# Optimization experiments

Measured on AMD Instinct MI355X. Metric: run time of the kernel, lower is better.

## Reference

```python
import math
import jax, jax.numpy as jnp
import numpy as np

N_HEAD = 12
LN_EPS = 1e-5

def _gelu(x):
    # NewGELU: tanh approximation
    c = math.sqrt(2.0 / math.pi)
    return 0.5 * x * (1.0 + jnp.tanh(c * (x + 0.044715 * x ** 3)))

def _ln(x, w, b):
    m = x.mean(-1, keepdims=True)
    v = x.var(-1, keepdims=True)
    return (x - m) / jnp.sqrt(v + LN_EPS) * w + b

def setup_inputs() -> dict:
    key = jax.random.key(0)
    ks = jax.random.split(key, 8)
    L, C, V, BS = 12, 768, 30522, 1024
    B, T = 4, 1024
    std = 0.02
    inp = {
        'idx': jax.random.randint(ks[0], (B, T), 0, V),
        'wte': jax.random.normal(ks[1], (V, C), jnp.float32) * std,
        'wpe': jax.random.normal(ks[2], (BS, C), jnp.float32) * std,
        'ln1_w': jnp.ones((L, C), jnp.float32),
        'ln1_b': jnp.zeros((L, C), jnp.float32),
        'attn_w': jax.random.normal(ks[3], (L, 3 * C, C), jnp.float32) * std,
        'attn_b': jnp.zeros((L, 3 * C), jnp.float32),
        'proj_w': jax.random.normal(ks[4], (L, C, C), jnp.float32) * (std / math.sqrt(2 * L)),
        'proj_b': jnp.zeros((L, C), jnp.float32),
        'ln2_w': jnp.ones((L, C), jnp.float32),
        'ln2_b': jnp.zeros((L, C), jnp.float32),
        'fc_w': jax.random.normal(ks[5], (L, 4 * C, C), jnp.float32) * std,
        'fc_b': jnp.zeros((L, 4 * C), jnp.float32),
        'mproj_w': jax.random.normal(ks[6], (L, C, 4 * C), jnp.float32) * (std / math.sqrt(2 * L)),
        'mproj_b': jnp.zeros((L, C), jnp.float32),
        'lnf_w': jnp.ones((C,), jnp.float32),
        'lnf_b': jnp.zeros((C,), jnp.float32),
        'lm_head_w': jax.random.normal(ks[7], (V, C), jnp.float32) * std,
    }
    return inp

def reference(idx, wte, wpe, ln1_w, ln1_b, attn_w, attn_b, proj_w, proj_b,
              ln2_w, ln2_b, fc_w, fc_b, mproj_w, mproj_b, lnf_w, lnf_b, lm_head_w):
    B, T = idx.shape
    C = wte.shape[1]
    H = N_HEAD
    D = C // H
    scale = 1.0 / math.sqrt(D)
    x = wte[idx] + wpe[:T][None]  # [B,T,C], drop is identity (p=0)

    def block(x, p):
        l1w, l1b, aw, ab, pw, pb, l2w, l2b, fw, fb, mw, mb = p
        h = _ln(x, l1w, l1b)
        qkv = jnp.einsum('btc,ec->bte', h, aw) + ab  # [B,T,3C]
        q, k, v = jnp.split(qkv, 3, axis=-1)
        q = q.reshape(B, T, H, D)
        k = k.reshape(B, T, H, D)
        v = v.reshape(B, T, H, D)
        att = jnp.einsum('bthd,bshd->bhts', q, k) * scale  # [B,H,T,T]
        att = jax.nn.softmax(att, axis=-1)  # mask=None: full attention
        y = jnp.einsum('bhts,bshd->bthd', att, v).reshape(B, T, C)
        x = x + jnp.einsum('btc,oc->bto', y, pw) + pb
        h = _gelu(jnp.einsum('btc,fc->btf', _ln(x, l2w, l2b), fw) + fb)
        x = x + jnp.einsum('btf,cf->btc', h, mw) + mb
        return x, None

    x, _ = jax.lax.scan(block, x, (ln1_w, ln1_b, attn_w, attn_b, proj_w, proj_b,
                                   ln2_w, ln2_b, fc_w, fc_b, mproj_w, mproj_b))
    x = _ln(x, lnf_w, lnf_b)
    logits = jnp.einsum('btc,vc->btv', x, lm_head_w)  # [B,T,V]
    return logits
```

## Files before the change

### kernel.cpp

```cpp
#include <hip/hip_runtime.h>
#include <hip/hip_bf16.h>
#include <math.h>

typedef __attribute__((ext_vector_type(8))) short short8;
typedef __attribute__((ext_vector_type(4))) float f32x4;

typedef unsigned short u16;

__device__ __forceinline__ u16 f2bf(float f) {
    union { float f; unsigned int u; } v; v.f = f;
    unsigned int u = v.u;
    unsigned int r = (u + 0x7fffu + ((u >> 16) & 1u)) >> 16;
    return (u16)r;
}
__device__ __forceinline__ float bf2f(u16 u) {
    union { unsigned int u; float f; } v; v.u = ((unsigned int)u) << 16;
    return v.f;
}

__device__ __forceinline__ void gload16(const void* g, void* l) {
    __builtin_amdgcn_global_load_lds(
        (const __attribute__((address_space(1))) void*)g,
        (__attribute__((address_space(3))) void*)l, 16, 0, 0);
}

__global__ __launch_bounds__(256) void castw_kernel(const float* __restrict__ src,
                                                    u16* __restrict__ dst,
                                                    long n, long npad) {
    long i = ((long)blockIdx.x * 256 + threadIdx.x) * 4;
    const long stride = (long)gridDim.x * 1024;
    for (; i < npad; i += stride) {
        ushort4 o;
        if (i < n) {
            float4 v = *reinterpret_cast<const float4*>(src + i);
            o.x = f2bf(v.x); o.y = f2bf(v.y); o.z = f2bf(v.z); o.w = f2bf(v.w);
        } else {
            o = make_ushort4(0, 0, 0, 0);
        }
        *reinterpret_cast<ushort4*>(dst + i) = o;
    }
}

__global__ __launch_bounds__(256) void embed_kernel(const int* __restrict__ idx,
                                                    const float* __restrict__ wte,
                                                    const float* __restrict__ wpe,
                                                    float* __restrict__ x) {
    const int row = blockIdx.x;
    const int tid = threadIdx.x;
    const int t = row & 1023;
    const int tok = idx[row];
    const float* we = wte + (size_t)tok * 768;
    const float* pe = wpe + (size_t)t * 768;
    float* xr = x + (size_t)row * 768;
    xr[tid]       = we[tid]       + pe[tid];
    xr[tid + 256] = we[tid + 256] + pe[tid + 256];
    xr[tid + 512] = we[tid + 512] + pe[tid + 512];
}

__global__ __launch_bounds__(256) void ln_kernel(const float* __restrict__ x,
                                                 const float* __restrict__ w,
                                                 const float* __restrict__ b,
                                                 u16* __restrict__ out) {
    const int row = blockIdx.x;
    const int tid = threadIdx.x;
    const float* xr = x + (size_t)row * 768;
    float v0 = xr[tid], v1 = xr[tid + 256], v2 = xr[tid + 512];
    float s = v0 + v1 + v2;
    float q = v0 * v0 + v1 * v1 + v2 * v2;
    #pragma unroll
    for (int off = 32; off >= 1; off >>= 1) {
        s += __shfl_xor(s, off);
        q += __shfl_xor(q, off);
    }
    __shared__ float rs[4], rq[4];
    const int wid = tid >> 6, lane = tid & 63;
    if (lane == 0) { rs[wid] = s; rq[wid] = q; }
    __syncthreads();
    s = rs[0] + rs[1] + rs[2] + rs[3];
    q = rq[0] + rq[1] + rq[2] + rq[3];
    const float mean = s * (1.f / 768.f);
    const float var = q * (1.f / 768.f) - mean * mean;
    const float rstd = rsqrtf(var + 1e-5f);
    u16* orow = out + (size_t)row * 768;
    orow[tid]       = f2bf((v0 - mean) * rstd * w[tid]       + b[tid]);
    orow[tid + 256] = f2bf((v1 - mean) * rstd * w[tid + 256] + b[tid + 256]);
    orow[tid + 512] = f2bf((v2 - mean) * rstd * w[tid + 512] + b[tid + 512]);
}

template<int EPI>
__global__ __launch_bounds__(256) void gemm_bb(
        const u16* __restrict__ A, int lda,
        const u16* __restrict__ B, int ldb,
        const float* __restrict__ bias,
        void* __restrict__ Cout, int ldc,
        int N, int K, int nmt,
        float* __restrict__ resid) {
    __shared__ __align__(16) u16 lds[2][2][128 * 32];
    const int tid = threadIdx.x;
    const int lane = tid & 63, wid = tid >> 6;
    const int nwg = gridDim.x;
    const int o = blockIdx.x;
    const int wg = (o & 7) * (nwg >> 3) + (o >> 3);
    const int m0 = (wg % nmt) * 128, n0 = (wg / nmt) * 128;

    const int wm = (wid >> 1) * 64, wn = (wid & 1) * 64;
    const int l16 = lane & 15, lk = (lane >> 4) * 8;

    const size_t a_off0 = (size_t)(m0 + (tid >> 2)) * lda + (tid & 3) * 8;
    const size_t a_off1 = a_off0 + (size_t)64 * lda;
    const size_t b_off0 = (size_t)(n0 + (tid >> 2)) * ldb + (tid & 3) * 8;
    const size_t b_off1 = b_off0 + (size_t)64 * ldb;

    f32x4 acc[4][4];
    #pragma unroll
    for (int i = 0; i < 4; i++)
        #pragma unroll
        for (int j = 0; j < 4; j++)
            acc[i][j] = (f32x4){0.f, 0.f, 0.f, 0.f};

    const int nk = K >> 5;
    {
        u16* As = lds[0][0]; u16* Bs = lds[0][1];
        gload16(A + a_off0, As + tid * 8);
        gload16(A + a_off1, As + tid * 8 + 2048);
        gload16(B + b_off0, Bs + tid * 8);
        gload16(B + b_off1, Bs + tid * 8 + 2048);
    }
    for (int t = 0; t < nk; ++t) {
        if (t + 1 < nk) {
            u16* As = lds[(t + 1) & 1][0]; u16* Bs = lds[(t + 1) & 1][1];
            const int k0 = (t + 1) << 5;
            gload16(A + a_off0 + k0, As + tid * 8);
            gload16(A + a_off1 + k0, As + tid * 8 + 2048);
            gload16(B + b_off0 + k0, Bs + tid * 8);
            gload16(B + b_off1 + k0, Bs + tid * 8 + 2048);
            asm volatile("s_waitcnt vmcnt(4)" ::: "memory");
        } else {
            asm volatile("s_waitcnt vmcnt(0)" ::: "memory");
        }
        __builtin_amdgcn_s_barrier();
        asm volatile("" ::: "memory");
        const u16* As = lds[t & 1][0];
        const u16* Bs = lds[t & 1][1];
        short8 af[4], bf[4];
        #pragma unroll
        for (int i = 0; i < 4; i++) {
            af[i] = *reinterpret_cast<const short8*>(&As[(wm + i * 16 + l16) * 32 + lk]);
            bf[i] = *reinterpret_cast<const short8*>(&Bs[(wn + i * 16 + l16) * 32 + lk]);
        }
        #pragma unroll
        for (int mi = 0; mi < 4; mi++)
            #pragma unroll
            for (int ni = 0; ni < 4; ni++)
                acc[mi][ni] = __builtin_amdgcn_mfma_f32_16x16x32_bf16(af[mi], bf[ni], acc[mi][ni], 0, 0, 0);
        asm volatile("" ::: "memory");
        __builtin_amdgcn_s_barrier();
    }

    if (EPI == 3) {
        float* ct = reinterpret_cast<float*>(&lds[0][0][0]) + wid * 1024;
        const int rw = (lane >> 4) * 4;
        const int rr = lane >> 2;
        const int rc = (lane & 3) * 16;
        #pragma unroll
        for (int mi = 0; mi < 4; mi++) {
            asm volatile("" ::: "memory");
            #pragma unroll
            for (int ni = 0; ni < 4; ni++)
                #pragma unroll
                for (int j = 0; j < 4; j++)
                    ct[(rw + j) * 64 + ni * 16 + l16] = acc[mi][ni][j];
            asm volatile("" ::: "memory");
            const int m = m0 + wm + mi * 16 + rr;
            const int nb = n0 + wn + rc;
            float* crow = (float*)Cout + (size_t)m * ldc + nb;
            #pragma unroll
            for (int q = 0; q < 4; q++) {
                const float4 v = *reinterpret_cast<const float4*>(&ct[rr * 64 + rc + q * 4]);
                if (nb + q * 4 + 3 < N) {
                    *reinterpret_cast<float4*>(crow + q * 4) = v;
                } else {
                    const float vv[4] = {v.x, v.y, v.z, v.w};
                    #pragma unroll
                    for (int e = 0; e < 4; e++)
                        if (nb + q * 4 + e < N) crow[q * 4 + e] = vv[e];
                }
            }
        }
    } else {
        const int cb = n0 + wn + l16;
        const int rb = m0 + wm + (lane >> 4) * 4;
        #pragma unroll
        for (int ni = 0; ni < 4; ni++) {
            const int n = cb + ni * 16;
            const float bv = bias[n];
            #pragma unroll
            for (int mi = 0; mi < 4; mi++) {
                #pragma unroll
                for (int j = 0; j < 4; j++) {
                    const int m = rb + mi * 16 + j;
                    float v = acc[mi][ni][j] + bv;
                    if (EPI == 0) {
                        ((u16*)Cout)[(size_t)m * ldc + n] = f2bf(v);
                    } else if (EPI == 1) {
                        resid[(size_t)m * ldc + n] += v;
                    } else {
                        const float t = tanhf(0.7978845608028654f * (v + 0.044715f * v * v * v));
                        ((u16*)Cout)[(size_t)m * ldc + n] = f2bf(0.5f * v * (1.f + t));
                    }
                }
            }
        }
    }
}

template<int EPI>
__global__ __launch_bounds__(256, 2) void gemm_bt(
        const u16* __restrict__ A, int lda,
        const float* __restrict__ B, int ldb,
        const float* __restrict__ bias,
        void* __restrict__ Cout, int ldc,
        int M, int N, int K,
        float* __restrict__ resid) {
    __shared__ __align__(16) u16 As[128][40];
    __shared__ __align__(16) u16 Bs[128][40];
    const int tid = threadIdx.x;
    const int lane = tid & 63, wid = tid >> 6;
    const int m0 = blockIdx.y * 128, n0 = blockIdx.x * 128;
    const int wm = (wid >> 1) * 64, wn = (wid & 1) * 64;
    const int l16 = lane & 15, lk = (lane >> 4) * 8;

    f32x4 acc[4][4];
    #pragma unroll
    for (int i = 0; i < 4; i++)
        #pragma unroll
        for (int j = 0; j < 4; j++)
            acc[i][j] = (f32x4){0.f, 0.f, 0.f, 0.f};

    for (int k0 = 0; k0 < K; k0 += 32) {
        #pragma unroll
        for (int p = 0; p < 2; p++) {
            const int e = p * 256 + tid;
            const int r = e >> 2, c = e & 3;
            uint4 v = *reinterpret_cast<const uint4*>(A + (size_t)(m0 + r) * lda + k0 + c * 8);
            *reinterpret_cast<uint4*>(&As[r][c * 8]) = v;
        }
        #pragma unroll
        for (int p = 0; p < 4; p++) {
            const int e = p * 256 + tid;
            const int r = e >> 3, c = e & 7;
            float4 v = make_float4(0.f, 0.f, 0.f, 0.f);
            if (n0 + r < N)
                v = *reinterpret_cast<const float4*>(B + (size_t)(n0 + r) * ldb + k0 + c * 4);
            ushort4 hv;
            hv.x = f2bf(v.x); hv.y = f2bf(v.y); hv.z = f2bf(v.z); hv.w = f2bf(v.w);
            *reinterpret_cast<ushort4*>(&Bs[r][c * 4]) = hv;
        }
        __syncthreads();
        short8 af[4], bfr[4];
        #pragma unroll
        for (int i = 0; i < 4; i++) {
            af[i]  = *reinterpret_cast<const short8*>(&As[wm + i * 16 + l16][lk]);
            bfr[i] = *reinterpret_cast<const short8*>(&Bs[wn + i * 16 + l16][lk]);
        }
        #pragma unroll
        for (int mi = 0; mi < 4; mi++)
            #pragma unroll
            for (int ni = 0; ni < 4; ni++)
                acc[mi][ni] = __builtin_amdgcn_mfma_f32_16x16x32_bf16(af[mi], bfr[ni], acc[mi][ni], 0, 0, 0);
        __syncthreads();
    }

    const int cb = n0 + wn + l16;
    const int rb = m0 + wm + (lane >> 4) * 4;
    #pragma unroll
    for (int ni = 0; ni < 4; ni++) {
        const int n = cb + ni * 16;
        if (n >= N) continue;
        float bv = 0.f;
        if (EPI != 3) bv = bias[n];
        #pragma unroll
        for (int mi = 0; mi < 4; mi++) {
            #pragma unroll
            for (int j = 0; j < 4; j++) {
                const int m = rb + mi * 16 + j;
                float v = acc[mi][ni][j] + bv;
                if (EPI == 0) {
                    ((u16*)Cout)[(size_t)m * ldc + n] = f2bf(v);
                } else if (EPI == 1) {
                    resid[(size_t)m * ldc + n] += v;
                } else if (EPI == 2) {
                    const float t = tanhf(0.7978845608028654f * (v + 0.044715f * v * v * v));
                    ((u16*)Cout)[(size_t)m * ldc + n] = f2bf(0.5f * v * (1.f + t));
                } else {
                    ((float*)Cout)[(size_t)m * ldc + n] = v;
                }
            }
        }
    }
}

__global__ __launch_bounds__(256, 2) void attn_mfma_kernel(const u16* __restrict__ qkv,
                                                           u16* __restrict__ y) {
    __shared__ __align__(16) u16 Qs[64][72];
    __shared__ __align__(16) u16 Ks[64][72];
    __shared__ __align__(16) u16 Vt[64][72];
    __shared__ __align__(16) u16 Ps[4][16][72];

    const int tid = threadIdx.x;
    const int lane = tid & 63, wid = tid >> 6;
    const int l16 = lane & 15, lk = (lane >> 4) * 8;
    const int qt = blockIdx.x, h = blockIdx.y, b = blockIdx.z;

    const size_t base = (size_t)b * 1024 * 2304;
    const u16* qp = qkv + base + (size_t)(qt * 64) * 2304 + h * 64;
    const u16* kp = qkv + base + 768  + h * 64;
    const u16* vp = qkv + base + 1536 + h * 64;

    #pragma unroll
    for (int p = 0; p < 2; p++) {
        const int e = p * 256 + tid;
        const int rr = e >> 3, c8 = e & 7;
        *reinterpret_cast<uint4*>(&Qs[rr][c8 * 8]) =
            *reinterpret_cast<const uint4*>(qp + (size_t)rr * 2304 + c8 * 8);
    }
    __syncthreads();

    short8 qf[2];
    #pragma unroll
    for (int kk = 0; kk < 2; kk++)
        qf[kk] = *reinterpret_cast<const short8*>(&Qs[wid * 16 + l16][kk * 32 + lk]);

    f32x4 o_acc[4];
    #pragma unroll
    for (int i = 0; i < 4; i++) o_acc[i] = (f32x4){0.f, 0.f, 0.f, 0.f};
    float l_part[4] = {0.f, 0.f, 0.f, 0.f};

    for (int s0 = 0; s0 < 1024; s0 += 64) {
        __syncthreads();
        #pragma unroll
        for (int p = 0; p < 2; p++) {
            const int e = p * 256 + tid;
            const int rr = e >> 3, c8 = e & 7;
            *reinterpret_cast<uint4*>(&Ks[rr][c8 * 8]) =
                *reinterpret_cast<const uint4*>(kp + (size_t)(s0 + rr) * 2304 + c8 * 8);
        }
        #pragma unroll
        for (int p = 0; p < 2; p++) {
            const int e = p * 256 + tid;
            const int s2 = e >> 4;
            const int dq = e & 15;
            const int s = s2 * 2;
            ushort4 v0 = *reinterpret_cast<const ushort4*>(vp + (size_t)(s0 + s) * 2304 + dq * 4);
            ushort4 v1 = *reinterpret_cast<const ushort4*>(vp + (size_t)(s0 + s + 1) * 2304 + dq * 4);
            *reinterpret_cast<ushort2*>(&Vt[dq * 4 + 0][s]) = make_ushort2(v0.x, v1.x);
            *reinterpret_cast<ushort2*>(&Vt[dq * 4 + 1][s]) = make_ushort2(v0.y, v1.y);
            *reinterpret_cast<ushort2*>(&Vt[dq * 4 + 2][s]) = make_ushort2(v0.z, v1.z);
            *reinterpret_cast<ushort2*>(&Vt[dq * 4 + 3][s]) = make_ushort2(v0.w, v1.w);
        }
        __syncthreads();

        f32x4 sa[4];
        #pragma unroll
        for (int i = 0; i < 4; i++) sa[i] = (f32x4){0.f, 0.f, 0.f, 0.f};
        #pragma unroll
        for (int nj = 0; nj < 4; nj++) {
            #pragma unroll
            for (int kk = 0; kk < 2; kk++) {
                short8 kf = *reinterpret_cast<const short8*>(&Ks[nj * 16 + l16][kk * 32 + lk]);
                sa[nj] = __builtin_amdgcn_mfma_f32_16x16x32_bf16(qf[kk], kf, sa[nj], 0, 0, 0);
            }
        }

        #pragma unroll
        for (int nj = 0; nj < 4; nj++) {
            #pragma unroll
            for (int r = 0; r < 4; r++) {
                const float pv = __expf(sa[nj][r] * 0.125f);
                l_part[r] += pv;
                Ps[wid][(lane >> 4) * 4 + r][nj * 16 + l16] = f2bf(pv);
            }
        }

        short8 pa[2];
        #pragma unroll
        for (int kk = 0; kk < 2; kk++)
            pa[kk] = *reinterpret_cast<const short8*>(&Ps[wid][l16][kk * 32 + lk]);
        #pragma unroll
        for (int nd = 0; nd < 4; nd++) {
            #pragma unroll
            for (int kk = 0; kk < 2; kk++) {
                short8 vf = *reinterpret_cast<const short8*>(&Vt[nd * 16 + l16][kk * 32 + lk]);
                o_acc[nd] = __builtin_amdgcn_mfma_f32_16x16x32_bf16(pa[kk], vf, o_acc[nd], 0, 0, 0);
            }
        }
    }

    float inv[4];
    #pragma unroll
    for (int r = 0; r < 4; r++) {
        float s = l_part[r];
        #pragma unroll
        for (int off = 8; off >= 1; off >>= 1) s += __shfl_xor(s, off);
        inv[r] = 1.f / s;
    }
    const int rowb = b * 1024 + qt * 64 + wid * 16 + (lane >> 4) * 4;
    #pragma unroll
    for (int nd = 0; nd < 4; nd++) {
        const int col = h * 64 + nd * 16 + l16;
        #pragma unroll
        for (int r = 0; r < 4; r++) {
            y[(size_t)(rowb + r) * 768 + col] = f2bf(o_acc[nd][r] * inv[r]);
        }
    }
}

extern "C" void kernel_launch(void* const* d_in, const int* in_sizes, int n_in,
                              void* d_out, int out_size, void* d_ws, size_t ws_size,
                              hipStream_t stream) {
    (void)in_sizes; (void)n_in; (void)out_size;
    const int*   idx    = (const int*)d_in[0];
    const float* wte    = (const float*)d_in[1];
    const float* wpe    = (const float*)d_in[2];
    const float* ln1w   = (const float*)d_in[3];
    const float* ln1b   = (const float*)d_in[4];
    const float* attnw  = (const float*)d_in[5];
    const float* attnb  = (const float*)d_in[6];
    const float* projw  = (const float*)d_in[7];
    const float* projb  = (const float*)d_in[8];
    const float* ln2w   = (const float*)d_in[9];
    const float* ln2b   = (const float*)d_in[10];
    const float* fcw    = (const float*)d_in[11];
    const float* fcb    = (const float*)d_in[12];
    const float* mprojw = (const float*)d_in[13];
    const float* mprojb = (const float*)d_in[14];
    const float* lnfw   = (const float*)d_in[15];
    const float* lnfb   = (const float*)d_in[16];
    const float* lmw    = (const float*)d_in[17];
    float* out = (float*)d_out;

    char* p = (char*)d_ws;
    size_t used = 0;
    auto take = [&](size_t bytes) { char* q = p + used; used += (bytes + 255) & ~(size_t)255; return q; };
    float* x      = (float*)take((size_t)4096 * 768 * 4);
    u16*   a_bf   = (u16*)take((size_t)4096 * 768 * 2);
    u16*   qkv_bf = (u16*)take((size_t)4096 * 2304 * 2);
    u16*   hid_bf = (u16*)take((size_t)4096 * 3072 * 2);
    u16*   w_lm   = (u16*)take((size_t)30592 * 768 * 2);
    const bool castLm = used <= ws_size;
    u16*   w_attn = (u16*)take((size_t)12 * 2304 * 768 * 2);
    u16*   w_proj = (u16*)take((size_t)12 * 768 * 768 * 2);
    u16*   w_fc   = (u16*)take((size_t)12 * 3072 * 768 * 2);
    u16*   w_mprj = (u16*)take((size_t)12 * 768 * 3072 * 2);
    const bool castAll = used <= ws_size;

    embed_kernel<<<4096, 256, 0, stream>>>(idx, wte, wpe, x);

    if (castLm)
        castw_kernel<<<2048, 256, 0, stream>>>(lmw, w_lm, (long)30522 * 768, (long)30592 * 768);
    if (castAll) {
        castw_kernel<<<2048, 256, 0, stream>>>(attnw,  w_attn, (long)12 * 2304 * 768, (long)12 * 2304 * 768);
        castw_kernel<<<2048, 256, 0, stream>>>(projw,  w_proj, (long)12 * 768 * 768,  (long)12 * 768 * 768);
        castw_kernel<<<2048, 256, 0, stream>>>(fcw,    w_fc,   (long)12 * 3072 * 768, (long)12 * 3072 * 768);
        castw_kernel<<<2048, 256, 0, stream>>>(mprojw, w_mprj, (long)12 * 768 * 3072, (long)12 * 768 * 3072);
    }

    for (int l = 0; l < 12; l++) {
        ln_kernel<<<4096, 256, 0, stream>>>(x, ln1w + l * 768, ln1b + l * 768, a_bf);
        if (castAll) {
            gemm_bb<0><<<32 * 18, 256, 0, stream>>>(
                a_bf, 768, w_attn + (size_t)l * 2304 * 768, 768, attnb + l * 2304,
                (void*)qkv_bf, 2304, 2304, 768, 32, nullptr);
        } else {
            gemm_bt<0><<<dim3(18, 32), 256, 0, stream>>>(
                a_bf, 768, attnw + (size_t)l * 2304 * 768, 768, attnb + l * 2304,
                (void*)qkv_bf, 2304, 4096, 2304, 768, nullptr);
        }
        attn_mfma_kernel<<<dim3(16, 12, 4), 256, 0, stream>>>(qkv_bf, a_bf);
        if (castAll) {
            gemm_bb<1><<<32 * 6, 256, 0, stream>>>(
                a_bf, 768, w_proj + (size_t)l * 768 * 768, 768, projb + l * 768,
                nullptr, 768, 768, 768, 32, x);
        } else {
            gemm_bt<1><<<dim3(6, 32), 256, 0, stream>>>(
                a_bf, 768, projw + (size_t)l * 768 * 768, 768, projb + l * 768,
                nullptr, 768, 4096, 768, 768, x);
        }
        ln_kernel<<<4096, 256, 0, stream>>>(x, ln2w + l * 768, ln2b + l * 768, a_bf);
        if (castAll) {
            gemm_bb<2><<<32 * 24, 256, 0, stream>>>(
                a_bf, 768, w_fc + (size_t)l * 3072 * 768, 768, fcb + l * 3072,
                (void*)hid_bf, 3072, 3072, 768, 32, nullptr);
            gemm_bb<1><<<32 * 6, 256, 0, stream>>>(
                hid_bf, 3072, w_mprj + (size_t)l * 768 * 3072, 3072, mprojb + l * 768,
                nullptr, 768, 768, 3072, 32, x);
        } else {
            gemm_bt<2><<<dim3(24, 32), 256, 0, stream>>>(
                a_bf, 768, fcw + (size_t)l * 3072 * 768, 768, fcb + l * 3072,
                (void*)hid_bf, 3072, 4096, 3072, 768, nullptr);
            gemm_bt<1><<<dim3(6, 32), 256, 0, stream>>>(
                hid_bf, 3072, mprojw + (size_t)l * 768 * 3072, 3072, mprojb + l * 768,
                nullptr, 768, 4096, 768, 3072, x);
        }
    }

    ln_kernel<<<4096, 256, 0, stream>>>(x, lnfw, lnfb, a_bf);
    if (castLm) {
        gemm_bb<3><<<32 * 239, 256, 0, stream>>>(
            a_bf, 768, w_lm, 768, nullptr, (void*)out, 30522, 30522, 768, 32, nullptr);
    } else {
        gemm_bt<3><<<dim3(239, 32), 256, 0, stream>>>(
            a_bf, 768, lmw, 768, nullptr, (void*)out, 30522, 4096, 30522, 768, nullptr);
    }
}
```

Measured before the change: 3.191 ms.

## Triple-buffer GEMM LDS tiles, raise MFMA priority, pad and nontemporal-store logits epilogue

The bf16 GEMM's LDS staging grows from double to triple buffering, so global loads are issued two k-steps ahead and waited with a deeper vmcnt. The MFMA block is wrapped in s_setprio to favour math issue. The fp32 logits epilogue now pads its LDS transpose stride to 68 floats to avoid bank conflicts and writes output with nontemporal stores to limit cache pollution from the large logits tensor. LDS use per block rises, which could reduce occupancy.

```diff
diff --git a/kernel.cpp b/kernel.cpp
--- a/kernel.cpp
+++ b/kernel.cpp
@@ -95,7 +95,8 @@
         void* __restrict__ Cout, int ldc,
         int N, int K, int nmt,
         float* __restrict__ resid) {
-    __shared__ __align__(16) u16 lds[2][2][128 * 32];
+    __shared__ __align__(16) u16 ldsA[3][128 * 32];
+    __shared__ __align__(16) u16 ldsB[3][128 * 32];
     const int tid = threadIdx.x;
     const int lane = tid & 63, wid = tid >> 6;
     const int nwg = gridDim.x;
@@ -110,6 +111,7 @@
     const size_t a_off1 = a_off0 + (size_t)64 * lda;
     const size_t b_off0 = (size_t)(n0 + (tid >> 2)) * ldb + (tid & 3) * 8;
     const size_t b_off1 = b_off0 + (size_t)64 * ldb;
+    const int ldst = tid * 8;
 
     f32x4 acc[4][4];
     #pragma unroll
@@ -119,46 +121,58 @@
             acc[i][j] = (f32x4){0.f, 0.f, 0.f, 0.f};
 
     const int nk = K >> 5;
-    {
-        u16* As = lds[0][0]; u16* Bs = lds[0][1];
-        gload16(A + a_off0, As + tid * 8);
-        gload16(A + a_off1, As + tid * 8 + 2048);
-        gload16(B + b_off0, Bs + tid * 8);
-        gload16(B + b_off1, Bs + tid * 8 + 2048);
-    }
+    gload16(A + a_off0, ldsA[0] + ldst);
+    gload16(A + a_off1, ldsA[0] + ldst + 2048);
+    gload16(B + b_off0, ldsB[0] + ldst);
+    gload16(B + b_off1, ldsB[0] + ldst + 2048);
+    if (nk > 1) {
+        gload16(A + a_off0 + 32, ldsA[1] + ldst);
+        gload16(A + a_off1 + 32, ldsA[1] + ldst + 2048);
+        gload16(B + b_off0 + 32, ldsB[1] + ldst);
+        gload16(B + b_off1 + 32, ldsB[1] + ldst + 2048);
+    }
+
+    int cc = 0, cp = 2;
     for (int t = 0; t < nk; ++t) {
-        if (t + 1 < nk) {
-            u16* As = lds[(t + 1) & 1][0]; u16* Bs = lds[(t + 1) & 1][1];
-            const int k0 = (t + 1) << 5;
-            gload16(A + a_off0 + k0, As + tid * 8);
-            gload16(A + a_off1 + k0, As + tid * 8 + 2048);
-            gload16(B + b_off0 + k0, Bs + tid * 8);
-            gload16(B + b_off1 + k0, Bs + tid * 8 + 2048);
+        if (t + 2 < nk) {
+            const int k0 = (t + 2) << 5;
+            u16* Ap = ldsA[0] + cp * (128 * 32);
+            u16* Bp = ldsB[0] + cp * (128 * 32);
+            gload16(A + a_off0 + k0, Ap + ldst);
+            gload16(A + a_off1 + k0, Ap + ldst + 2048);
+            gload16(B + b_off0 + k0, Bp + ldst);
+            gload16(B + b_off1 + k0, Bp + ldst + 2048);
+            asm volatile("s_waitcnt vmcnt(8)" ::: "memory");
+        } else if (t + 1 < nk) {
             asm volatile("s_waitcnt vmcnt(4)" ::: "memory");
         } else {
             asm volatile("s_waitcnt vmcnt(0)" ::: "memory");
         }
         __builtin_amdgcn_s_barrier();
         asm volatile("" ::: "memory");
-        const u16* As = lds[t & 1][0];
-        const u16* Bs = lds[t & 1][1];
+        const u16* As = ldsA[0] + cc * (128 * 32);
+        const u16* Bs = ldsB[0] + cc * (128 * 32);
         short8 af[4], bf[4];
         #pragma unroll
         for (int i = 0; i < 4; i++) {
             af[i] = *reinterpret_cast<const short8*>(&As[(wm + i * 16 + l16) * 32 + lk]);
             bf[i] = *reinterpret_cast<const short8*>(&Bs[(wn + i * 16 + l16) * 32 + lk]);
         }
+        __builtin_amdgcn_s_setprio(1);
         #pragma unroll
         for (int mi = 0; mi < 4; mi++)
             #pragma unroll
             for (int ni = 0; ni < 4; ni++)
                 acc[mi][ni] = __builtin_amdgcn_mfma_f32_16x16x32_bf16(af[mi], bf[ni], acc[mi][ni], 0, 0, 0);
+        __builtin_amdgcn_s_setprio(0);
         asm volatile("" ::: "memory");
         __builtin_amdgcn_s_barrier();
+        cc = (cc == 2) ? 0 : cc + 1;
+        cp = (cp == 2) ? 0 : cp + 1;
     }
 
     if (EPI == 3) {
-        float* ct = reinterpret_cast<float*>(&lds[0][0][0]) + wid * 1024;
+        float* ct = reinterpret_cast<float*>(&ldsA[0][0]) + wid * 1088;
         const int rw = (lane >> 4) * 4;
         const int rr = lane >> 2;
         const int rc = (lane & 3) * 16;
@@ -169,21 +183,20 @@
             for (int ni = 0; ni < 4; ni++)
                 #pragma unroll
                 for (int j = 0; j < 4; j++)
-                    ct[(rw + j) * 64 + ni * 16 + l16] = acc[mi][ni][j];
+                    ct[(rw + j) * 68 + ni * 16 + l16] = acc[mi][ni][j];
             asm volatile("" ::: "memory");
             const int m = m0 + wm + mi * 16 + rr;
             const int nb = n0 + wn + rc;
             float* crow = (float*)Cout + (size_t)m * ldc + nb;
             #pragma unroll
             for (int q = 0; q < 4; q++) {
-                const float4 v = *reinterpret_cast<const float4*>(&ct[rr * 64 + rc + q * 4]);
+                const f32x4 v = *reinterpret_cast<const f32x4*>(&ct[rr * 68 + rc + q * 4]);
                 if (nb + q * 4 + 3 < N) {
-                    *reinterpret_cast<float4*>(crow + q * 4) = v;
+                    __builtin_nontemporal_store(v, reinterpret_cast<f32x4*>(crow + q * 4));
                 } else {
-                    const float vv[4] = {v.x, v.y, v.z, v.w};
                     #pragma unroll
                     for (int e = 0; e < 4; e++)
-                        if (nb + q * 4 + e < N) crow[q * 4 + e] = vv[e];
+                        if (nb + q * 4 + e < N) crow[q * 4 + e] = v[e];
                 }
             }
         }
```

Result: slower. 4.106 ms (+28.7%).
